# Kernel tuning notes

Measured on AMD Instinct MI355X. Metric: run time of the kernel, lower is better.

Reference implementation:

```python
import jax, jax.numpy as jnp
import numpy as np

H, HK, D, W = 16, 4, 128, 512   # heads, kv heads, head dim, window size
SCALE = D ** -0.5
T = 8192


def setup_inputs() -> dict:
    key = jax.random.key(0)
    k1, k2, k3 = jax.random.split(key, 3)
    return {
        "query": jax.random.normal(k1, (T, H * D), dtype=jnp.float32),
        "key": jax.random.normal(k2, (T, HK * D), dtype=jnp.float32),
        "value": jax.random.normal(k3, (T, HK * D), dtype=jnp.float32),
    }


def reference(query, key, value):
    """Causal sliding-window attention (window W, incl. self) returning (out, lse).

    Banded formulation: queries are split into blocks of size W; each block
    attends only to its own block and the previous block, so the full [T,T]
    score matrix is never materialized.
    """
    Tn = query.shape[0]
    nb = Tn // W
    G = H // HK  # query heads per kv head
    q = query.reshape(nb, W, HK, G, D)
    k = key.reshape(nb, W, HK, D)
    v = value.reshape(nb, W, HK, D)
    # previous block of keys/values (zeros before block 0, masked out below)
    k_prev = jnp.concatenate([jnp.zeros_like(k[:1]), k[:-1]], axis=0)
    v_prev = jnp.concatenate([jnp.zeros_like(v[:1]), v[:-1]], axis=0)
    kk = jnp.concatenate([k_prev, k], axis=1)  # [nb, 2W, HK, D]
    vv = jnp.concatenate([v_prev, v], axis=1)
    # scores: [nb, HK, G, W, 2W]
    s = jnp.einsum('nqhgd,nkhd->nhgqk', q, kk) * SCALE
    i = jnp.arange(W)[:, None]       # local query pos
    j = jnp.arange(2 * W)[None, :]   # local key pos; key_abs - q_abs = j - W - i
    in_win = (j >= i + 1) & (j <= i + W)        # W keys ending at self
    b_idx = jnp.arange(nb)[:, None, None]
    valid = in_win[None] & ((b_idx > 0) | (j[None] >= W))  # block 0 has no prev keys
    s = jnp.where(valid[:, None, None], s, jnp.finfo(s.dtype).min)
    s32 = s.astype(jnp.float32)
    lse = jax.nn.logsumexp(s32, axis=-1)          # [nb, HK, G, W]
    p = jnp.exp(s32 - lse[..., None]).astype(q.dtype)
    o = jnp.einsum('nhgqk,nkhd->nqhgd', p, vv)
    out = o.reshape(Tn, H * D)
    lse_out = lse.transpose(1, 2, 0, 3).reshape(H, Tn)  # head h = hk*G + g
    return out, lse_out
```

## Files before the change

### kernel.cpp

```cpp
#include <hip/hip_runtime.h>
#include <hip/hip_bf16.h>


#define T_SEQ 8192
#define H_Q   16
#define HK_KV 4
#define D_HD  128
#define W_WIN 512
#define SCL2E 0.12753785397738803f
#define LN2   0.6931471805599453f

typedef __bf16 bf16_t;
typedef bf16_t bf16x8 __attribute__((ext_vector_type(8)));
typedef float  f32x4  __attribute__((ext_vector_type(4)));
typedef ushort us8    __attribute__((ext_vector_type(8)));

union U4 { uint2 u; bf16_t b[4]; };

__device__ inline bf16x8 to_bf8(float4 a, float4 b) {
    bf16x8 r;
    r[0] = (bf16_t)a.x; r[1] = (bf16_t)a.y; r[2] = (bf16_t)a.z; r[3] = (bf16_t)a.w;
    r[4] = (bf16_t)b.x; r[5] = (bf16_t)b.y; r[6] = (bf16_t)b.z; r[7] = (bf16_t)b.w;
    return r;
}

__device__ __forceinline__ void gld16(const void* g, void* l) {
    __builtin_amdgcn_global_load_lds(
        (const __attribute__((address_space(1))) void*)g,
        (__attribute__((address_space(3))) void*)l, 16, 0, 0);
}

__global__ __launch_bounds__(256) void prep_kv(const float* __restrict__ key,
                                               const float* __restrict__ val,
                                               bf16_t* __restrict__ Kb,
                                               bf16_t* __restrict__ Vt) {
    __shared__ ushort tile[64][68];
    const int tid = threadIdx.x;
    if (blockIdx.x < 4096) {
        int e = ((int)blockIdx.x * 256 + tid) * 4;
        int t  = e >> 9;
        int c  = e & 511;
        int hk = c >> 7;
        int d  = c & 127;
        float4 v = *(const float4*)(key + e);
        U4 p;
        p.b[0] = (bf16_t)v.x; p.b[1] = (bf16_t)v.y; p.b[2] = (bf16_t)v.z; p.b[3] = (bf16_t)v.w;
        *(uint2*)(void*)(Kb + ((size_t)hk * T_SEQ + t) * 128 + d) = p.u;
        return;
    }
    int b   = blockIdx.x - 4096;
    int hk  = b >> 8;
    int rem = b & 255;
    int t0  = (rem & 127) << 6;
    int d0  = (rem >> 7) << 6;

    int i  = tid >> 2;
    int j0 = (tid & 3) << 4;
    const float* src = val + (size_t)(t0 + i) * 512 + hk * 128 + d0 + j0;
#pragma unroll
    for (int k = 0; k < 4; ++k) {
        float4 v = *(const float4*)(src + 4 * k);
        U4 p;
        p.b[0] = (bf16_t)v.x; p.b[1] = (bf16_t)v.y; p.b[2] = (bf16_t)v.z; p.b[3] = (bf16_t)v.w;
        *(uint2*)(void*)&tile[i][j0 + 4 * k] = p.u;
    }
    __syncthreads();
    int dd8 = tid >> 3;
    int tq  = (tid & 7) << 3;
#pragma unroll
    for (int half = 0; half < 2; ++half) {
        int dd = half * 32 + dd8;
        us8 u;
#pragma unroll
        for (int j = 0; j < 8; ++j) u[j] = tile[tq + j][dd];
        bf16_t* dst = Vt + ((size_t)hk * 128 + d0 + dd) * T_SEQ + t0 + tq;
        *(us8*)(void*)dst = u;
    }
}

__global__ __launch_bounds__(256) void attn_main(const float* __restrict__ qg,
                                                 const bf16_t* __restrict__ Kb,
                                                 const bf16_t* __restrict__ Vt,
                                                 float* __restrict__ out) {
    __shared__ ushort Kls[2][4096] __attribute__((aligned(16)));
    __shared__ ushort Vls[2][4096] __attribute__((aligned(16)));
    __shared__ ushort Plds[4][16][40] __attribute__((aligned(16)));

    const int bid = blockIdx.x;
    const int w   = (bid & 7) * 256 + (bid >> 3);
    const int h   = w >> 7;
    const int qb  = w & 127;
    const int hk  = h >> 2;
    const int tid  = threadIdx.x;
    const int wv   = tid >> 6;
    const int lane = tid & 63;
    const int lq   = lane & 15;
    const int g    = lane >> 4;
    const int q0b  = qb * 64;
    const int q0w  = q0b + wv * 16;
    const int qa   = q0w + lq;

    bf16x8 qf[4];
    const float* qp = qg + (size_t)qa * 2048 + h * 128 + 8 * g;
#pragma unroll
    for (int kc = 0; kc < 4; ++kc) {
        float4 a = *(const float4*)(qp + kc * 32);
        float4 b = *(const float4*)(qp + kc * 32 + 4);
        qf[kc] = to_bf8(a, b);
    }

    f32x4 acc[8];
#pragma unroll
    for (int i = 0; i < 8; ++i) acc[i] = (f32x4){0.f, 0.f, 0.f, 0.f};
    float mrun = -1e4f;
    float lsum = 0.f;

    const bf16_t* kb_ = Kb + (size_t)hk * T_SEQ * 128;
    const bf16_t* vb_ = Vt + (size_t)hk * 128 * T_SEQ;

    const int lob  = q0b - (W_WIN - 1);
    const int ktb0 = lob > 0 ? (lob >> 5) : 0;
    const int ktb1 = (q0b + 63) >> 5;
    const int wlow = q0w - (W_WIN - 1);
    const int bq   = 4 * g - qa + 511;

    const uint okg0 = ((uint)(tid >> 4)) * 128 + (uint)(((tid & 15) ^ ((tid >> 4) & 7)) << 3);
    const uint ovg0 = ((uint)(tid >> 2)) * T_SEQ + (uint)(((tid & 3) ^ ((tid >> 3) & 3)) << 3);
    char* const ldsK0 = (char*)&Kls[0][0] + tid * 16;
    char* const ldsK1 = (char*)&Kls[1][0] + tid * 16;
    char* const ldsV0 = (char*)&Vls[0][0] + tid * 16;
    char* const ldsV1 = (char*)&Vls[1][0] + tid * 16;

    const uint e6  = (lane & 4) << 4;
    const uint blo = (uint)((g * 16) ^ ((lq & 3) << 4));
    const char* kbA_e = (const char*)&Kls[0][0] + lq * 256 + blo + e6;
    const char* kbA_o = (const char*)&Kls[0][0] + lq * 256 + blo + (64 - e6);
    const char* kbB_e = (const char*)&Kls[1][0] + lq * 256 + blo + e6;
    const char* kbB_o = (const char*)&Kls[1][0] + lq * 256 + blo + (64 - e6);
    const uint vswz = (uint)((g ^ ((lq >> 1) & 3)) << 4);
    const char* vbA = (const char*)&Vls[0][0] + lq * 64 + vswz;
    const char* vbB = (const char*)&Vls[1][0] + lq * 64 + vswz;

    ushort* const pw0 = &Plds[wv][lq][4 * g];
    ushort* const pw1 = pw0 + 16;
    const ushort* const prd = &Plds[wv][lq][8 * g];

    auto stage = [&](char* lk, char* lv, int kbs_) {
        const bf16_t* kt_ = kb_ + (size_t)kbs_ * 128;
        const bf16_t* vt_ = vb_ + kbs_;
        gld16(kt_ + okg0,          lk);
        gld16(kt_ + 2048 + okg0,   lk + 4096);
        gld16(vt_ + ovg0,          lv);
        gld16(vt_ + 524288 + ovg0, lv + 4096);
    };

    auto compute = [&](const char* kbe, const char* kbo, const char* vbp, int kbs_) {
        if (kbs_ + 31 < wlow || kbs_ > q0w + 15) return;

        f32x4 s0 = {0.f, 0.f, 0.f, 0.f}, s1 = {0.f, 0.f, 0.f, 0.f};
        __builtin_amdgcn_s_setprio(1);
#pragma unroll
        for (int kc = 0; kc < 4; ++kc) {
            const char* pa = (kc & 1) ? kbo : kbe;
            const int  off = (kc >> 1) * 128;
            bf16x8 k0 = *(const bf16x8*)(pa + off);
            bf16x8 k1 = *(const bf16x8*)(pa + off + 4096);
            s0 = __builtin_amdgcn_mfma_f32_16x16x32_bf16(k0, qf[kc], s0, 0, 0, 0);
            s1 = __builtin_amdgcn_mfma_f32_16x16x32_bf16(k1, qf[kc], s1, 0, 0, 0);
        }
        __builtin_amdgcn_s_setprio(0);

        float sv[8];
        const bool interior = (kbs_ >= q0w - 496) && (kbs_ + 31 <= q0w);
        if (interior) {
#pragma unroll
            for (int r = 0; r < 4; ++r) { sv[r] = s0[r]; sv[4 + r] = s1[r]; }
        } else {
            const int b0 = kbs_ + bq;
#pragma unroll
            for (int r = 0; r < 4; ++r) {
                sv[r]     = ((uint)(b0 + r)      <= 511u) ? s0[r] : -1e30f;
                sv[4 + r] = ((uint)(b0 + 16 + r) <= 511u) ? s1[r] : -1e30f;
            }
        }

        float tm = sv[0];
#pragma unroll
        for (int i = 1; i < 8; ++i) tm = fmaxf(tm, sv[i]);
        tm = fmaxf(tm, __shfl_xor(tm, 16));
        tm = fmaxf(tm, __shfl_xor(tm, 32));
        const float tms = tm * SCL2E;

        if (!__all(tms <= mrun + 11.54f)) {
            float mnew  = fmaxf(mrun, tms);
            float alpha = __builtin_amdgcn_exp2f(mrun - mnew);
            lsum *= alpha;
#pragma unroll
            for (int i = 0; i < 8; ++i) acc[i] *= alpha;
            mrun = mnew;
        }

        float p[8];
        float ps = 0.f;
#pragma unroll
        for (int i = 0; i < 8; ++i) {
            p[i] = __builtin_amdgcn_exp2f(fmaf(sv[i], SCL2E, -mrun));
            ps += p[i];
        }
        ps += __shfl_xor(ps, 16);
        ps += __shfl_xor(ps, 32);
        lsum += ps;

        U4 w0, w1;
        w0.b[0] = (bf16_t)p[0]; w0.b[1] = (bf16_t)p[1]; w0.b[2] = (bf16_t)p[2]; w0.b[3] = (bf16_t)p[3];
        w1.b[0] = (bf16_t)p[4]; w1.b[1] = (bf16_t)p[5]; w1.b[2] = (bf16_t)p[6]; w1.b[3] = (bf16_t)p[7];
        *(uint2*)(void*)pw0 = w0.u;
        *(uint2*)(void*)pw1 = w1.u;
        asm volatile("s_waitcnt lgkmcnt(0)" ::: "memory");
        bf16x8 pb = *(const bf16x8*)(const void*)prd;

        __builtin_amdgcn_s_setprio(1);
#pragma unroll
        for (int dt = 0; dt < 8; ++dt) {
            bf16x8 vf = *(const bf16x8*)(vbp + dt * 1024);
            acc[dt] = __builtin_amdgcn_mfma_f32_16x16x32_bf16(vf, pb, acc[dt], 0, 0, 0);
        }
        __builtin_amdgcn_s_setprio(0);
    };

    stage(ldsK0, ldsV0, ktb0 << 5);
    __syncthreads();

    int kt = ktb0;
    while (kt + 1 <= ktb1) {
        stage(ldsK1, ldsV1, (kt + 1) << 5);
        compute(kbA_e, kbA_o, vbA, kt << 5);
        __syncthreads();
        if (kt + 2 <= ktb1) stage(ldsK0, ldsV0, (kt + 2) << 5);
        compute(kbB_e, kbB_o, vbB, (kt + 1) << 5);
        __syncthreads();
        kt += 2;
    }
    if (kt <= ktb1) compute(kbA_e, kbA_o, vbA, kt << 5);

    float inv = 1.0f / lsum;
#pragma unroll
    for (int dt = 0; dt < 8; ++dt) {
        float4 o;
        o.x = acc[dt][0] * inv; o.y = acc[dt][1] * inv;
        o.z = acc[dt][2] * inv; o.w = acc[dt][3] * inv;
        *(float4*)(out + (size_t)qa * 2048 + h * 128 + dt * 16 + 4 * g) = o;
    }
    if (lane < 16) {
        out[(size_t)T_SEQ * 2048 + (size_t)h * T_SEQ + qa] =
            LN2 * (mrun + log2f(lsum));
    }
}

extern "C" void kernel_launch(void* const* d_in, const int* in_sizes, int n_in,
                              void* d_out, int out_size, void* d_ws, size_t ws_size,
                              hipStream_t stream) {
    const float* q = (const float*)d_in[0];
    const float* k = (const float*)d_in[1];
    const float* v = (const float*)d_in[2];
    float* out = (float*)d_out;

    bf16_t* Kb = (bf16_t*)d_ws;
    bf16_t* Vt = Kb + (size_t)HK_KV * T_SEQ * D_HD;

    prep_kv<<<4096 + HK_KV * (T_SEQ / 64) * (D_HD / 64), 256, 0, stream>>>(k, v, Kb, Vt);
    attn_main<<<(T_SEQ / 64) * H_Q, 256, 0, stream>>>(q, Kb, Vt, out);
}
```

Measured before the change: 209.9 us.

## Use partial vmcnt waits in K/V double buffer and swizzle P LDS layout

Result: no change. 213.6 us (+1.8%).

```diff
diff --git a/kernel.cpp b/kernel.cpp
--- a/kernel.cpp
+++ b/kernel.cpp
@@ -141,9 +141,11 @@
     const char* vbA = (const char*)&Vls[0][0] + lq * 64 + vswz;
     const char* vbB = (const char*)&Vls[1][0] + lq * 64 + vswz;
 
-    ushort* const pw0 = &Plds[wv][lq][4 * g];
-    ushort* const pw1 = pw0 + 16;
-    const ushort* const prd = &Plds[wv][lq][8 * g];
+    const int  b3x2 = (lq >> 3) << 1;
+    const int  p1   = (g >> 1) ^ b3x2;
+    ushort* const pw0 = &Plds[wv][lq][p1 * 8 + (g & 1) * 4];
+    ushort* const pw1 = &Plds[wv][lq][(p1 ^ 2) * 8 + (g & 1) * 4];
+    const ushort* const prd = &Plds[wv][lq][(g ^ b3x2) * 8];
 
     auto stage = [&](char* lk, char* lv, int kbs_) {
         const bf16_t* kt_ = kb_ + (size_t)kbs_ * 128;
@@ -217,6 +219,7 @@
         *(uint2*)(void*)pw0 = w0.u;
         *(uint2*)(void*)pw1 = w1.u;
         asm volatile("s_waitcnt lgkmcnt(0)" ::: "memory");
+        __builtin_amdgcn_sched_barrier(0);
         bf16x8 pb = *(const bf16x8*)(const void*)prd;
 
         __builtin_amdgcn_s_setprio(1);
@@ -229,19 +232,33 @@
     };
 
     stage(ldsK0, ldsV0, ktb0 << 5);
-    __syncthreads();
-
     int kt = ktb0;
-    while (kt + 1 <= ktb1) {
-        stage(ldsK1, ldsV1, (kt + 1) << 5);
+    for (;;) {
+        asm volatile("" ::: "memory");
+        __builtin_amdgcn_s_barrier();
+        if (kt < ktb1) {
+            stage(ldsK1, ldsV1, (kt + 1) << 5);
+            asm volatile("s_waitcnt vmcnt(4)" ::: "memory");
+        } else {
+            asm volatile("s_waitcnt vmcnt(0)" ::: "memory");
+        }
+        __builtin_amdgcn_s_barrier();
+        __builtin_amdgcn_sched_barrier(0);
         compute(kbA_e, kbA_o, vbA, kt << 5);
-        __syncthreads();
-        if (kt + 2 <= ktb1) stage(ldsK0, ldsV0, (kt + 2) << 5);
-        compute(kbB_e, kbB_o, vbB, (kt + 1) << 5);
-        __syncthreads();
-        kt += 2;
-    }
-    if (kt <= ktb1) compute(kbA_e, kbA_o, vbA, kt << 5);
+        if (++kt > ktb1) break;
+        asm volatile("" ::: "memory");
+        __builtin_amdgcn_s_barrier();
+        if (kt < ktb1) {
+            stage(ldsK0, ldsV0, (kt + 1) << 5);
+            asm volatile("s_waitcnt vmcnt(4)" ::: "memory");
+        } else {
+            asm volatile("s_waitcnt vmcnt(0)" ::: "memory");
+        }
+        __builtin_amdgcn_s_barrier();
+        __builtin_amdgcn_sched_barrier(0);
+        compute(kbB_e, kbB_o, vbB, kt << 5);
+        if (++kt > ktb1) break;
+    }
 
     float inv = 1.0f / lsum;
 #pragma unroll
```
